# Performance work log

Hardware: AMD Instinct MI355X
Metric: run time of the kernel (lower is better)

Reference implementation:

```python
import jax, jax.numpy as jnp
import numpy as np

B, S, D = 2, 2048, 2048
H, HKV, HD = 16, 4, 128
GROUPS = H // HKV
SCALE = HD ** -0.5
ROPE_THETA = 10000.0
NEG = -1e9


def _rope_cos_sin():
    inv_freq = 1.0 / (ROPE_THETA ** (jnp.arange(0, HD, 2, dtype=jnp.float32) / HD))  # [HD/2]
    pos = jnp.arange(S, dtype=jnp.float32)
    freqs = pos[:, None] * inv_freq[None, :]            # [S, HD/2]
    emb = jnp.concatenate([freqs, freqs], axis=-1)      # [S, HD]
    cos = jnp.broadcast_to(jnp.cos(emb)[None], (B, S, HD))
    sin = jnp.broadcast_to(jnp.sin(emb)[None], (B, S, HD))
    return cos, sin


def setup_inputs() -> dict:
    key = jax.random.key(0)
    ks = jax.random.split(key, 5)
    hidden_states = jax.random.normal(ks[0], (B, S, D), dtype=jnp.float32)
    cos, sin = _rope_cos_sin()
    causal = jnp.where(jnp.arange(S)[:, None] >= jnp.arange(S)[None, :], 0.0, NEG).astype(jnp.float32)
    attn_mask = jnp.broadcast_to(causal[None, None], (B, 1, S, S))
    wq = jax.random.normal(ks[1], (H * HD, D), dtype=jnp.float32) * (D ** -0.5)
    wk = jax.random.normal(ks[2], (HKV * HD, D), dtype=jnp.float32) * (D ** -0.5)
    wv = jax.random.normal(ks[3], (HKV * HD, D), dtype=jnp.float32) * (D ** -0.5)
    wo = jax.random.normal(ks[4], (D, H * HD), dtype=jnp.float32) * (D ** -0.5)
    return {"hidden_states": hidden_states, "cos": cos, "sin": sin,
            "attn_mask": attn_mask, "wq": wq, "wk": wk, "wv": wv, "wo": wo}


def _rotate_half(x):
    x1, x2 = x[..., : HD // 2], x[..., HD // 2:]
    return jnp.concatenate([-x2, x1], axis=-1)


def reference(hidden_states, cos, sin, attn_mask, wq, wk, wv, wo):
    # projections (torch Linear: x @ W.T), reshape to [B, heads, S, HD]
    q = (hidden_states @ wq.T).reshape(B, S, H, HD).transpose(0, 2, 1, 3)
    k = (hidden_states @ wk.T).reshape(B, S, HKV, HD).transpose(0, 2, 1, 3)
    v = (hidden_states @ wv.T).reshape(B, S, HKV, HD).transpose(0, 2, 1, 3)
    # RoPE (cos/sin broadcast over head dim)
    c = cos[:, None, :, :]
    s = sin[:, None, :, :]
    q = q * c + _rotate_half(q) * s
    k = k * c + _rotate_half(k) * s
    # GQA: repeat each kv head GROUPS times consecutively (matches repeat_kv)
    k = jnp.repeat(k, GROUPS, axis=1)
    v = jnp.repeat(v, GROUPS, axis=1)
    logits = jnp.einsum('bhqd,bhkd->bhqk', q, k) * SCALE + attn_mask
    w = jax.nn.softmax(logits.astype(jnp.float32), axis=-1).astype(q.dtype)
    out = jnp.einsum('bhqk,bhkd->bhqd', w, v)            # [B,H,S,HD]
    out = out.transpose(0, 2, 1, 3).reshape(B, S, H * HD)
    return out @ wo.T
```

## Files before the change

kernel.cpp:

```cpp
#include <hip/hip_runtime.h>

typedef __attribute__((ext_vector_type(8))) short bf16x8;
typedef __attribute__((ext_vector_type(4))) float f32x4;
typedef __attribute__((ext_vector_type(16))) float f32x16;
typedef __attribute__((ext_vector_type(8))) unsigned short u16x8;
typedef __attribute__((ext_vector_type(4))) unsigned u32x4;
typedef unsigned short u16;

#define GLOBAL_AS __attribute__((address_space(1)))
#define LDS_AS __attribute__((address_space(3)))

#define S_ 2048
#define SMK_ 0.12751741406106783f

static __device__ __forceinline__ u16 f2bf(float f) {
  unsigned u = __builtin_bit_cast(unsigned, f);
  u += 0x7fffu + ((u >> 16) & 1u);
  return (u16)(u >> 16);
}
static __device__ __forceinline__ float bf2f(u16 h) {
  return __builtin_bit_cast(float, ((unsigned)h) << 16);
}
static __device__ __forceinline__ float exp2_raw(float x) {
  float r; asm("v_exp_f32 %0, %1" : "=v"(r) : "v"(x)); return r;
}
static __device__ __forceinline__ unsigned cvtpk(float lo, float hi_) {
  unsigned r; asm("v_cvt_pk_bf16_f32 %0, %1, %2" : "=v"(r) : "v"(lo), "v"(hi_)); return r;
}
static __device__ __forceinline__ float tmax16(const f32x16& s) {
  float a0 = fmaxf(s[0], s[1]),  a1 = fmaxf(s[2], s[3]);
  float a2 = fmaxf(s[4], s[5]),  a3 = fmaxf(s[6], s[7]);
  float a4 = fmaxf(s[8], s[9]),  a5 = fmaxf(s[10], s[11]);
  float a6 = fmaxf(s[12], s[13]), a7 = fmaxf(s[14], s[15]);
  return fmaxf(fmaxf(fmaxf(a0, a1), fmaxf(a2, a3)),
               fmaxf(fmaxf(a4, a5), fmaxf(a6, a7)));
}
static __device__ __forceinline__ float tsum16(const f32x16& s) {
  float a0 = s[0] + s[1],  a1 = s[2] + s[3];
  float a2 = s[4] + s[5],  a3 = s[6] + s[7];
  float a4 = s[8] + s[9],  a5 = s[10] + s[11];
  float a6 = s[12] + s[13], a7 = s[14] + s[15];
  return ((a0 + a1) + (a2 + a3)) + ((a4 + a5) + (a6 + a7));
}

__global__ __launch_bounds__(256)
void cvt_all(const float* __restrict__ h, const float* __restrict__ wq,
             const float* __restrict__ wk, const float* __restrict__ wv,
             const float* __restrict__ wo, u16* __restrict__ Xbf,
             u16* __restrict__ Wqkv, u16* __restrict__ Wo) {
  const int bid = blockIdx.x;
  const float* src; u16* dst; long base;
  if (bid < 4096)      { src = h;  dst = Xbf;            base = (long)bid * 2048; }
  else if (bid < 6144) { src = wq; dst = Wqkv;           base = (long)(bid - 4096) * 2048; }
  else if (bid < 6656) { src = wk; dst = Wqkv + 4194304; base = (long)(bid - 6144) * 2048; }
  else if (bid < 7168) { src = wv; dst = Wqkv + 5242880; base = (long)(bid - 6656) * 2048; }
  else                 { src = wo; dst = Wo;             base = (long)(bid - 7168) * 2048; }
  const long i = base + (long)threadIdx.x * 8;
  f32x4 a = *(const f32x4*)(src + i);
  f32x4 b = *(const f32x4*)(src + i + 4);
  u16x8 o;
  o[0] = f2bf(a[0]); o[1] = f2bf(a[1]); o[2] = f2bf(a[2]); o[3] = f2bf(a[3]);
  o[4] = f2bf(b[0]); o[5] = f2bf(b[1]); o[6] = f2bf(b[2]); o[7] = f2bf(b[3]);
  *(u16x8*)(dst + i) = o;
}

template <int NJ, bool BF16OUT>
__global__ __launch_bounds__(512, 2)
void gemm256(const u16* __restrict__ A, const u16* __restrict__ Bw,
             void* __restrict__ Cp, int M, int N, int K) {
  __shared__ u16 LA[4][2][4096];
  __shared__ u16 LB[4][NJ / 2][4096];

  const int tid = threadIdx.x;
  const int wave = tid >> 6, lane = tid & 63;
  const int fr = lane & 15, fg = lane >> 4;
  const int wm = (wave >> 2) * 128;
  const int wn = (wave & 3) * (NJ * 16);
  const long rowA = (long)blockIdx.y * 256;
  const long rowB = (long)blockIdx.x * (NJ * 64);

  const int srow = tid >> 2;
  const int sc8 = (tid & 3) ^ (srow & 3);
  const int wbase = wave * 512;

  const int nt = K >> 5;

  f32x4 acc[8][NJ] = {};

#define STAGE_A(pt)                                                          \
  {                                                                          \
    const int _b = (pt) & 3;                                                 \
    const long _k = (long)(pt) * 32 + sc8 * 8;                               \
    __builtin_amdgcn_global_load_lds(                                        \
        (GLOBAL_AS void*)(A + (rowA + srow) * K + _k),                       \
        (LDS_AS void*)(&LA[_b][0][wbase]), 16, 0, 0);                        \
    __builtin_amdgcn_global_load_lds(                                        \
        (GLOBAL_AS void*)(A + (rowA + 128 + srow) * K + _k),                 \
        (LDS_AS void*)(&LA[_b][1][wbase]), 16, 0, 0);                        \
  }
#define STAGE_B(pt)                                                          \
  {                                                                          \
    const int _b = (pt) & 3;                                                 \
    const long _k = (long)(pt) * 32 + sc8 * 8;                               \
    __builtin_amdgcn_global_load_lds(                                        \
        (GLOBAL_AS void*)(Bw + (rowB + srow) * K + _k),                      \
        (LDS_AS void*)(&LB[_b][0][wbase]), 16, 0, 0);                        \
    if (NJ == 4)                                                             \
      __builtin_amdgcn_global_load_lds(                                      \
          (GLOBAL_AS void*)(Bw + (rowB + 128 + srow) * K + _k),              \
          (LDS_AS void*)(&LB[_b][NJ / 2 - 1][wbase]), 16, 0, 0);             \
  }

  STAGE_A(0); STAGE_B(0);
  STAGE_A(1); STAGE_B(1);
  STAGE_A(2); STAGE_B(2);

  for (int t = 0; t < nt; ++t) {
    const int rem = nt - 1 - t;
    if (NJ == 4) {
      if (rem >= 2)      asm volatile("s_waitcnt vmcnt(8)" ::: "memory");
      else if (rem == 1) asm volatile("s_waitcnt vmcnt(4)" ::: "memory");
      else               asm volatile("s_waitcnt vmcnt(0)" ::: "memory");
    } else {
      if (rem >= 2)      asm volatile("s_waitcnt vmcnt(6)" ::: "memory");
      else if (rem == 1) asm volatile("s_waitcnt vmcnt(3)" ::: "memory");
      else               asm volatile("s_waitcnt vmcnt(0)" ::: "memory");
    }
    __builtin_amdgcn_s_barrier();

    const u16* Ah = LA[t & 3][wm >> 7];
    const u16* Bh = LB[t & 3][NJ == 4 ? (wn >> 7) : 0];
    const bool pf = (t + 3) < nt;

    bf16x8 af0[4], bfv[NJ];
#pragma unroll
    for (int mi = 0; mi < 4; ++mi) {
      const int rl = mi * 16 + fr;
      af0[mi] = *(const bf16x8*)&Ah[rl * 32 + ((fg ^ (rl & 3)) << 3)];
    }
#pragma unroll
    for (int nj = 0; nj < NJ; ++nj) {
      const int rb = (wn & 127) + nj * 16 + fr;
      bfv[nj] = *(const bf16x8*)&Bh[rb * 32 + ((fg ^ (rb & 3)) << 3)];
    }
    if (pf) STAGE_A(t + 3);
    __builtin_amdgcn_s_setprio(1);
#pragma unroll
    for (int mi = 0; mi < 4; ++mi)
#pragma unroll
      for (int nj = 0; nj < NJ; ++nj)
        acc[mi][nj] = __builtin_amdgcn_mfma_f32_16x16x32_bf16(af0[mi], bfv[nj], acc[mi][nj], 0, 0, 0);
    __builtin_amdgcn_s_setprio(0);

    bf16x8 af1[4];
#pragma unroll
    for (int mi = 0; mi < 4; ++mi) {
      const int rl = 64 + mi * 16 + fr;
      af1[mi] = *(const bf16x8*)&Ah[rl * 32 + ((fg ^ (rl & 3)) << 3)];
    }
    if (pf) STAGE_B(t + 3);
    __builtin_amdgcn_s_setprio(1);
#pragma unroll
    for (int mi = 0; mi < 4; ++mi)
#pragma unroll
      for (int nj = 0; nj < NJ; ++nj)
        acc[4 + mi][nj] = __builtin_amdgcn_mfma_f32_16x16x32_bf16(af1[mi], bfv[nj], acc[4 + mi][nj], 0, 0, 0);
    __builtin_amdgcn_s_setprio(0);

    __builtin_amdgcn_s_barrier();
  }
#undef STAGE_A
#undef STAGE_B

#pragma unroll
  for (int mi = 0; mi < 8; ++mi)
#pragma unroll
    for (int nj = 0; nj < NJ; ++nj)
#pragma unroll
      for (int r = 0; r < 4; ++r) {
        const long row = rowA + wm + mi * 16 + fg * 4 + r;
        const long col = rowB + wn + nj * 16 + fr;
        if (BF16OUT) ((u16*)Cp)[row * N + col] = f2bf(acc[mi][nj][r]);
        else         ((float*)Cp)[row * N + col] = acc[mi][nj][r];
      }
}

__global__ __launch_bounds__(256)
void rope_rearrange(const u16* __restrict__ QKV, const float* __restrict__ cosb,
                    const float* __restrict__ sinb, u16* __restrict__ Qr,
                    u16* __restrict__ Kr) {
  const int m = blockIdx.x;
  const int b = m >> 11, s = m & 2047;
  const int t = threadIdx.x;
  const u16* row = QKV + (long)m * 3072;
  const float* cp = cosb + (long)m * 128;
  const float* sp = sinb + (long)m * 128;
#pragma unroll
  for (int i = 0; i < 4; ++i) {
    const int idx = i * 256 + t;
    const int h = idx >> 6, d = idx & 63;
    const float x1 = bf2f(row[h * 128 + d]);
    const float x2 = bf2f(row[h * 128 + d + 64]);
    const float c = cp[d], sv = sp[d];
    const long o = ((long)(b * 16 + h) * S_ + s) * 128 + d;
    Qr[o] = f2bf(x1 * c - x2 * sv);
    Qr[o + 64] = f2bf(x2 * c + x1 * sv);
  }
  {
    const int h = t >> 6, d = t & 63;
    const float x1 = bf2f(row[2048 + h * 128 + d]);
    const float x2 = bf2f(row[2048 + h * 128 + d + 64]);
    const float c = cp[d], sv = sp[d];
    const long o = ((long)(b * 4 + h) * S_ + s) * 128 + d;
    Kr[o] = f2bf((x1 * c - x2 * sv) * SMK_);
    Kr[o + 64] = f2bf((x2 * c + x1 * sv) * SMK_);
  }
}

__global__ __launch_bounds__(256)
void transpose_v(const u16* __restrict__ QKV, u16* __restrict__ Vt) {
  __shared__ u16 t[32][33];
  const int s0 = blockIdx.x * 32, d0 = blockIdx.y * 32;
  const int bk = blockIdx.z;
  const int b = bk >> 2, kh = bk & 3;
  const int tx = threadIdx.x & 31, ty = threadIdx.x >> 5;
  const u16* src = QKV + 2560 + (long)kh * 128;
#pragma unroll
  for (int i = 0; i < 4; ++i) {
    const int sl = ty + i * 8;
    t[sl][tx] = src[(long)(b * S_ + s0 + sl) * 3072 + d0 + tx];
  }
  __syncthreads();
  u16* dst = Vt + (long)(b * 4 + kh) * 128 * S_;
#pragma unroll
  for (int i = 0; i < 4; ++i) {
    const int dl = ty + i * 8;
    dst[(long)(d0 + dl) * S_ + s0 + tx] = t[tx][dl];
  }
}

struct PA2 { bf16x8 a, b; };
static __device__ __forceinline__ PA2 pack_half(const f32x16 s) {
  PA2 out;
#pragma unroll
  for (int ks2 = 0; ks2 < 2; ++ks2) {
    const int rb = ks2 * 8;
    unsigned w0 = cvtpk(s[rb + 0], s[rb + 1]);
    unsigned w1 = cvtpk(s[rb + 2], s[rb + 3]);
    unsigned w2 = cvtpk(s[rb + 4], s[rb + 5]);
    unsigned w3 = cvtpk(s[rb + 6], s[rb + 7]);
    asm("v_permlane32_swap_b32 %0, %1" : "+v"(w0), "+v"(w2));
    asm("v_permlane32_swap_b32 %0, %1" : "+v"(w1), "+v"(w3));
    u32x4 pw; pw[0] = w0; pw[1] = w1; pw[2] = w2; pw[3] = w3;
    if (ks2 == 0) out.a = __builtin_bit_cast(bf16x8, pw);
    else          out.b = __builtin_bit_cast(bf16x8, pw);
  }
  return out;
}

template <int NH>
static __device__ __forceinline__ void attn_tile(
    const u16* __restrict__ Ks, const u16* __restrict__ Vs,
    const bf16x8 (&qf)[8], f32x16 (&acc)[4], float& m_run, float& l_run,
    const int kv0, const int qwmin, const int qg, const int l31,
    const int hi, const int r7) {
  f32x16 s[NH];
#pragma unroll
  for (int hh = 0; hh < NH; ++hh) s[hh] = (f32x16){};
  __builtin_amdgcn_s_setprio(1);
#pragma unroll
  for (int ds = 0; ds < 8; ++ds) {
    const int ch = ((2 * ds + hi) ^ r7) << 3;
#pragma unroll
    for (int hh = 0; hh < NH; ++hh) {
      const bf16x8 ka = *(const bf16x8*)&Ks[(hh * 32 + l31) * 128 + ch];
      s[hh] = __builtin_amdgcn_mfma_f32_32x32x16_bf16(ka, qf[ds], s[hh], 0, 0, 0);
    }
  }
  __builtin_amdgcn_s_setprio(0);

  if (kv0 + NH * 32 - 1 > qwmin) {
#pragma unroll
    for (int hh = 0; hh < NH; ++hh)
#pragma unroll
      for (int r = 0; r < 16; ++r) {
        const int cr = (r & 3) + 8 * (r >> 2) + 4 * hi;
        if (kv0 + hh * 32 + cr > qg) s[hh][r] = -3.0e38f;
      }
  }

  float mx = tmax16(s[0]);
  if (NH == 2) mx = fmaxf(mx, tmax16(s[1]));
  mx = fmaxf(mx, __shfl_xor(mx, 32));

  if (__any(mx > m_run + 8.0f)) {
    const float mn = fmaxf(m_run, mx);
    const float scq = exp2_raw(m_run - mn);
    m_run = mn; l_run *= scq;
#pragma unroll
    for (int r = 0; r < 16; ++r) {
      const int cr = (r & 3) + 8 * (r >> 2) + 4 * hi;
      const float sr = __shfl(scq, cr);
      acc[0][r] *= sr; acc[1][r] *= sr; acc[2][r] *= sr; acc[3][r] *= sr;
    }
  }

#pragma unroll
  for (int hh = 0; hh < NH; ++hh)
#pragma unroll
    for (int r = 0; r < 16; ++r) s[hh][r] = exp2_raw(s[hh][r] - m_run);
  float rs = tsum16(s[0]);
  if (NH == 2) rs += tsum16(s[1]);
  rs += __shfl_xor(rs, 32);
  l_run += rs;

  bf16x8 pa[2 * NH];
#pragma unroll
  for (int hh = 0; hh < NH; ++hh) {
    const PA2 p = pack_half(s[hh]);
    pa[2 * hh] = p.a; pa[2 * hh + 1] = p.b;
  }
  __builtin_amdgcn_s_setprio(1);
#pragma unroll
  for (int nj = 0; nj < 4; ++nj) {
    const int vrow = (nj * 32 + l31) * 64;
#pragma unroll
    for (int ks = 0; ks < 2 * NH; ++ks) {
      const bf16x8 vf = *(const bf16x8*)&Vs[vrow + (((2 * ks + hi) ^ r7) << 3)];
      acc[nj] = __builtin_amdgcn_mfma_f32_32x32x16_bf16(pa[ks], vf, acc[nj], 0, 0, 0);
    }
  }
  __builtin_amdgcn_s_setprio(0);
}

#define NUNITS 1024
__global__ __launch_bounds__(128)
void attn_fwd(const u16* __restrict__ Qr, const u16* __restrict__ Kr,
              const u16* __restrict__ Vt, u16* __restrict__ Att,
              unsigned* __restrict__ ctr) {
  __shared__ u16 Ks[64 * 128];
  __shared__ u16 Vs[128 * 64];
  __shared__ unsigned s_uid;

  const int tid = threadIdx.x, wave = tid >> 6, lane = tid & 63;
  const int l31 = lane & 31, hi = lane >> 5, r7 = lane & 7;

  for (;;) {
    __syncthreads();
    if (tid == 0) s_uid = atomicAdd(ctr, 1u);
    __syncthreads();
    const unsigned uid = s_uid;
    if (uid >= NUNITS) break;

    const int g = uid & 7;
    const int rem = uid >> 3;
    const int qt = 31 - (rem >> 2);
    const int b = g >> 2, kh = g & 3;
    const int h = kh * 4 + (rem & 3);
    const int qwmin = qt * 64 + wave * 32;

    const u16* Qb = Qr + (long)(b * 16 + h) * S_ * 128;
    const u16* Kb = Kr + (long)(b * 4 + kh) * S_ * 128;
    const u16* Vg = Vt + (long)(b * 4 + kh) * 128 * (long)S_;

    bf16x8 qf[8];
    const u16* qrow = Qb + (long)(qwmin + l31) * 128 + hi * 8;
#pragma unroll
    for (int ds = 0; ds < 8; ++ds) qf[ds] = *(const bf16x8*)(qrow + ds * 16);

    f32x16 acc[4] = {};
    float m_run = -1e30f, l_run = 0.f;
    const int qg = qwmin + l31;

    const int ntiles = qt + 1;
    for (int t = 0; t < ntiles; ++t) {
      const int kv0 = t * 64;
      __syncthreads();
#pragma unroll
      for (int c = 0; c < 8; ++c) {
        const int slab = wave * 8 + c;
        const int offu = slab * 512 + lane * 8;
        const int kvl = offu >> 7;
        const int kc = ((offu >> 3) & 15) ^ (kvl & 7);
        __builtin_amdgcn_global_load_lds(
            (GLOBAL_AS void*)(Kb + (long)(kv0 + kvl) * 128 + kc * 8),
            (LDS_AS void*)(Ks + slab * 512), 16, 0, 0);
        const int dr = offu >> 6;
        const int vc = ((offu >> 3) & 7) ^ (dr & 7);
        __builtin_amdgcn_global_load_lds(
            (GLOBAL_AS void*)(Vg + (long)dr * S_ + kv0 + vc * 8),
            (LDS_AS void*)(Vs + slab * 512), 16, 0, 0);
      }
      __syncthreads();

      if (kv0 + 32 <= qwmin + 31)
        attn_tile<2>(Ks, Vs, qf, acc, m_run, l_run, kv0, qwmin, qg, l31, hi, r7);
      else if (kv0 <= qwmin + 31)
        attn_tile<1>(Ks, Vs, qf, acc, m_run, l_run, kv0, qwmin, qg, l31, hi, r7);
    }

    const float inv = 1.0f / l_run;
#pragma unroll
    for (int r = 0; r < 16; ++r) {
      const int cr = (r & 3) + 8 * (r >> 2) + 4 * hi;
      const float ir = __shfl(inv, cr);
      const long orow = ((long)b * S_ + qt * 64 + wave * 32 + cr) * 2048 + h * 128 + l31;
      Att[orow]      = f2bf(acc[0][r] * ir);
      Att[orow + 32] = f2bf(acc[1][r] * ir);
      Att[orow + 64] = f2bf(acc[2][r] * ir);
      Att[orow + 96] = f2bf(acc[3][r] * ir);
    }
  }
}

extern "C" void kernel_launch(void* const* d_in, const int* in_sizes, int n_in,
                              void* d_out, int out_size, void* d_ws, size_t ws_size,
                              hipStream_t stream) {
  const float* hidden = (const float*)d_in[0];
  const float* cosb = (const float*)d_in[1];
  const float* sinb = (const float*)d_in[2];
  const float* wq = (const float*)d_in[4];
  const float* wk = (const float*)d_in[5];
  const float* wv = (const float*)d_in[6];
  const float* wo = (const float*)d_in[7];
  float* out = (float*)d_out;

  u16* Xbf  = (u16*)d_ws;
  u16* Wqkv = Xbf + 8388608;
  u16* Wo   = Wqkv + 6291456;
  u16* QKV  = Wo + 4194304;
  u16* Qr   = QKV + 12582912;
  u16* Kr   = Qr + 8388608;
  u16* Vtp  = Kr + 2097152;
  u16* Att  = Xbf;
  if (ws_size < (size_t)44040192 * 2) return;

  cvt_all<<<dim3(9216), dim3(256), 0, stream>>>(hidden, wq, wk, wv, wo, Xbf, Wqkv, Wo);
  gemm256<4, true><<<dim3(12, 16), dim3(512), 0, stream>>>(Xbf, Wqkv, (void*)QKV, 4096, 3072, 2048);
  rope_rearrange<<<dim3(4096), dim3(256), 0, stream>>>(QKV, cosb, sinb, Qr, Kr);
  transpose_v<<<dim3(64, 4, 8), dim3(256), 0, stream>>>(QKV, Vtp);
  hipMemsetAsync((void*)Wqkv, 0, 4, stream);
  attn_fwd<<<dim3(1024), dim3(128), 0, stream>>>(Qr, Kr, Vtp, Att, (unsigned*)Wqkv);
  gemm256<2, false><<<dim3(16, 16), dim3(512), 0, stream>>>(Att, Wo, (void*)out, 4096, 2048, 2048);
}
```

Baseline: 227.2 us.

## Use per-XCD work queues and 4-wave blocks sharing K/V tiles across head pairs

Replaces the single global work counter with eight per-(batch, kv-head) counters. Each block starts on the queue matching its XCC id, read via s_getreg, and falls back to the other queues when its own is empty, so K/V for a given kv head tends to stay in one XCD's L2. Blocks grow to 256 threads so two query heads sharing a kv head reuse each staged K/V tile in LDS, which halves the per-wave load work. The risks are coarser work units that may hurt load balance on the causal tail, and more atomic traffic when queues run dry.

```diff
diff --git a/kernel.cpp b/kernel.cpp
--- a/kernel.cpp
+++ b/kernel.cpp
@@ -333,11 +333,11 @@
   __builtin_amdgcn_s_setprio(0);
 }
 
-#define NUNITS 1024
-__global__ __launch_bounds__(128)
+#define PAIRS_PER_GRP 64u
+__global__ __launch_bounds__(256)
 void attn_fwd(const u16* __restrict__ Qr, const u16* __restrict__ Kr,
               const u16* __restrict__ Vt, u16* __restrict__ Att,
-              unsigned* __restrict__ ctr) {
+              unsigned* __restrict__ ctrs) {
   __shared__ u16 Ks[64 * 128];
   __shared__ u16 Vs[128 * 64];
   __shared__ unsigned s_uid;
@@ -345,19 +345,31 @@
   const int tid = threadIdx.x, wave = tid >> 6, lane = tid & 63;
   const int l31 = lane & 31, hi = lane >> 5, r7 = lane & 7;
 
+  const int xcc = __builtin_amdgcn_s_getreg(6164) & 7;
+
   for (;;) {
     __syncthreads();
-    if (tid == 0) s_uid = atomicAdd(ctr, 1u);
+    if (tid == 0) {
+      unsigned got = 0xffffffffu;
+#pragma unroll
+      for (int k = 0; k < 8; ++k) {
+        const int sq = (xcc + k) & 7;
+        const unsigned v = atomicAdd(&ctrs[sq], 1u);
+        if (v < PAIRS_PER_GRP) { got = (unsigned)sq * PAIRS_PER_GRP + v; break; }
+      }
+      s_uid = got;
+    }
     __syncthreads();
     const unsigned uid = s_uid;
-    if (uid >= NUNITS) break;
-
-    const int g = uid & 7;
-    const int rem = uid >> 3;
-    const int qt = 31 - (rem >> 2);
+    if (uid == 0xffffffffu) break;
+
+    const int g = uid >> 6;
+    const int u = uid & 63;
+    const int qt = 31 - (u >> 1);
+    const int hp = u & 1;
     const int b = g >> 2, kh = g & 3;
-    const int h = kh * 4 + (rem & 3);
-    const int qwmin = qt * 64 + wave * 32;
+    const int h = kh * 4 + hp * 2 + (wave >> 1);
+    const int qwmin = qt * 64 + (wave & 1) * 32;
 
     const u16* Qb = Qr + (long)(b * 16 + h) * S_ * 128;
     const u16* Kb = Kr + (long)(b * 4 + kh) * S_ * 128;
@@ -377,8 +389,8 @@
       const int kv0 = t * 64;
       __syncthreads();
 #pragma unroll
-      for (int c = 0; c < 8; ++c) {
-        const int slab = wave * 8 + c;
+      for (int c = 0; c < 4; ++c) {
+        const int slab = wave * 4 + c;
         const int offu = slab * 512 + lane * 8;
         const int kvl = offu >> 7;
         const int kc = ((offu >> 3) & 15) ^ (kvl & 7);
@@ -404,7 +416,7 @@
     for (int r = 0; r < 16; ++r) {
       const int cr = (r & 3) + 8 * (r >> 2) + 4 * hi;
       const float ir = __shfl(inv, cr);
-      const long orow = ((long)b * S_ + qt * 64 + wave * 32 + cr) * 2048 + h * 128 + l31;
+      const long orow = ((long)b * S_ + qwmin + cr) * 2048 + h * 128 + l31;
       Att[orow]      = f2bf(acc[0][r] * ir);
       Att[orow + 32] = f2bf(acc[1][r] * ir);
       Att[orow + 64] = f2bf(acc[2][r] * ir);
@@ -439,7 +451,7 @@
   gemm256<4, true><<<dim3(12, 16), dim3(512), 0, stream>>>(Xbf, Wqkv, (void*)QKV, 4096, 3072, 2048);
   rope_rearrange<<<dim3(4096), dim3(256), 0, stream>>>(QKV, cosb, sinb, Qr, Kr);
   transpose_v<<<dim3(64, 4, 8), dim3(256), 0, stream>>>(QKV, Vtp);
-  hipMemsetAsync((void*)Wqkv, 0, 4, stream);
-  attn_fwd<<<dim3(1024), dim3(128), 0, stream>>>(Qr, Kr, Vtp, Att, (unsigned*)Wqkv);
+  hipMemsetAsync((void*)Wqkv, 0, 32, stream);
+  attn_fwd<<<dim3(512), dim3(256), 0, stream>>>(Qr, Kr, Vtp, Att, (unsigned*)Wqkv);
   gemm256<2, false><<<dim3(16, 16), dim3(512), 0, stream>>>(Att, Wo, (void*)out, 4096, 2048, 2048);
 }
```

Result: slower. 257.4 us (+13.3%).

## Load K/V directly from global into registers in single-wave attention blocks

Applied to the files above, without the earlier changes.

The attention kernel drops LDS staging and the persistent atomic work queue. Each 64-thread block now handles one 32-row query strip and reads K and V fragments straight from global memory into registers, relying on cache reuse across the four heads sharing a KV head. This removes barriers and LDS traffic and allows higher occupancy via launch bounds. The cost is redundant global/L2 reads, and static scheduling in place of dynamic load balancing across the causal triangle.

```diff
diff --git a/kernel.cpp b/kernel.cpp
--- a/kernel.cpp
+++ b/kernel.cpp
@@ -259,25 +259,34 @@
 }
 
 template <int NH>
-static __device__ __forceinline__ void attn_tile(
-    const u16* __restrict__ Ks, const u16* __restrict__ Vs,
+static __device__ __forceinline__ void attn_tile_g(
+    const u16* __restrict__ Kb, const u16* __restrict__ Vg,
     const bf16x8 (&qf)[8], f32x16 (&acc)[4], float& m_run, float& l_run,
-    const int kv0, const int qwmin, const int qg, const int l31,
-    const int hi, const int r7) {
+    const int kv0, const int qwmin, const int qg, const int l31, const int hi) {
   f32x16 s[NH];
 #pragma unroll
   for (int hh = 0; hh < NH; ++hh) s[hh] = (f32x16){};
-  __builtin_amdgcn_s_setprio(1);
-#pragma unroll
-  for (int ds = 0; ds < 8; ++ds) {
-    const int ch = ((2 * ds + hi) ^ r7) << 3;
-#pragma unroll
-    for (int hh = 0; hh < NH; ++hh) {
-      const bf16x8 ka = *(const bf16x8*)&Ks[(hh * 32 + l31) * 128 + ch];
-      s[hh] = __builtin_amdgcn_mfma_f32_32x32x16_bf16(ka, qf[ds], s[hh], 0, 0, 0);
-    }
-  }
-  __builtin_amdgcn_s_setprio(0);
+  const u16* kr0 = Kb + (long)(kv0 + l31) * 128 + hi * 8;
+  {
+    bf16x8 ka[8];
+#pragma unroll
+    for (int ds = 0; ds < 8; ++ds) ka[ds] = *(const bf16x8*)(kr0 + ds * 16);
+    __builtin_amdgcn_s_setprio(1);
+#pragma unroll
+    for (int ds = 0; ds < 8; ++ds)
+      s[0] = __builtin_amdgcn_mfma_f32_32x32x16_bf16(ka[ds], qf[ds], s[0], 0, 0, 0);
+    __builtin_amdgcn_s_setprio(0);
+  }
+  if (NH == 2) {
+    bf16x8 ka[8];
+#pragma unroll
+    for (int ds = 0; ds < 8; ++ds) ka[ds] = *(const bf16x8*)(kr0 + 32 * 128 + ds * 16);
+    __builtin_amdgcn_s_setprio(1);
+#pragma unroll
+    for (int ds = 0; ds < 8; ++ds)
+      s[NH - 1] = __builtin_amdgcn_mfma_f32_32x32x16_bf16(ka[ds], qf[ds], s[NH - 1], 0, 0, 0);
+    __builtin_amdgcn_s_setprio(0);
+  }
 
   if (kv0 + NH * 32 - 1 > qwmin) {
 #pragma unroll
@@ -320,96 +329,71 @@
     const PA2 p = pack_half(s[hh]);
     pa[2 * hh] = p.a; pa[2 * hh + 1] = p.b;
   }
+
   __builtin_amdgcn_s_setprio(1);
 #pragma unroll
   for (int nj = 0; nj < 4; ++nj) {
-    const int vrow = (nj * 32 + l31) * 64;
-#pragma unroll
-    for (int ks = 0; ks < 2 * NH; ++ks) {
-      const bf16x8 vf = *(const bf16x8*)&Vs[vrow + (((2 * ks + hi) ^ r7) << 3)];
-      acc[nj] = __builtin_amdgcn_mfma_f32_32x32x16_bf16(pa[ks], vf, acc[nj], 0, 0, 0);
+    const u16* vr = Vg + (long)(nj * 32 + l31) * S_ + kv0 + hi * 8;
+    const bf16x8 vf0 = *(const bf16x8*)(vr);
+    const bf16x8 vf1 = *(const bf16x8*)(vr + 16);
+    acc[nj] = __builtin_amdgcn_mfma_f32_32x32x16_bf16(pa[0], vf0, acc[nj], 0, 0, 0);
+    acc[nj] = __builtin_amdgcn_mfma_f32_32x32x16_bf16(pa[1], vf1, acc[nj], 0, 0, 0);
+    if (NH == 2) {
+      const bf16x8 vf2 = *(const bf16x8*)(vr + 32);
+      const bf16x8 vf3 = *(const bf16x8*)(vr + 48);
+      acc[nj] = __builtin_amdgcn_mfma_f32_32x32x16_bf16(pa[2 * NH - 2], vf2, acc[nj], 0, 0, 0);
+      acc[nj] = __builtin_amdgcn_mfma_f32_32x32x16_bf16(pa[2 * NH - 1], vf3, acc[nj], 0, 0, 0);
     }
   }
   __builtin_amdgcn_s_setprio(0);
 }
 
-#define NUNITS 1024
-__global__ __launch_bounds__(128)
+__global__ __launch_bounds__(64, 3)
 void attn_fwd(const u16* __restrict__ Qr, const u16* __restrict__ Kr,
-              const u16* __restrict__ Vt, u16* __restrict__ Att,
-              unsigned* __restrict__ ctr) {
-  __shared__ u16 Ks[64 * 128];
-  __shared__ u16 Vs[128 * 64];
-  __shared__ unsigned s_uid;
-
-  const int tid = threadIdx.x, wave = tid >> 6, lane = tid & 63;
-  const int l31 = lane & 31, hi = lane >> 5, r7 = lane & 7;
-
-  for (;;) {
-    __syncthreads();
-    if (tid == 0) s_uid = atomicAdd(ctr, 1u);
-    __syncthreads();
-    const unsigned uid = s_uid;
-    if (uid >= NUNITS) break;
-
-    const int g = uid & 7;
-    const int rem = uid >> 3;
-    const int qt = 31 - (rem >> 2);
-    const int b = g >> 2, kh = g & 3;
-    const int h = kh * 4 + (rem & 3);
-    const int qwmin = qt * 64 + wave * 32;
-
-    const u16* Qb = Qr + (long)(b * 16 + h) * S_ * 128;
-    const u16* Kb = Kr + (long)(b * 4 + kh) * S_ * 128;
-    const u16* Vg = Vt + (long)(b * 4 + kh) * 128 * (long)S_;
-
-    bf16x8 qf[8];
-    const u16* qrow = Qb + (long)(qwmin + l31) * 128 + hi * 8;
-#pragma unroll
-    for (int ds = 0; ds < 8; ++ds) qf[ds] = *(const bf16x8*)(qrow + ds * 16);
-
-    f32x16 acc[4] = {};
-    float m_run = -1e30f, l_run = 0.f;
-    const int qg = qwmin + l31;
-
-    const int ntiles = qt + 1;
-    for (int t = 0; t < ntiles; ++t) {
-      const int kv0 = t * 64;
-      __syncthreads();
-#pragma unroll
-      for (int c = 0; c < 8; ++c) {
-        const int slab = wave * 8 + c;
-        const int offu = slab * 512 + lane * 8;
-        const int kvl = offu >> 7;
-        const int kc = ((offu >> 3) & 15) ^ (kvl & 7);
-        __builtin_amdgcn_global_load_lds(
-            (GLOBAL_AS void*)(Kb + (long)(kv0 + kvl) * 128 + kc * 8),
-            (LDS_AS void*)(Ks + slab * 512), 16, 0, 0);
-        const int dr = offu >> 6;
-        const int vc = ((offu >> 3) & 7) ^ (dr & 7);
-        __builtin_amdgcn_global_load_lds(
-            (GLOBAL_AS void*)(Vg + (long)dr * S_ + kv0 + vc * 8),
-            (LDS_AS void*)(Vs + slab * 512), 16, 0, 0);
-      }
-      __syncthreads();
-
-      if (kv0 + 32 <= qwmin + 31)
-        attn_tile<2>(Ks, Vs, qf, acc, m_run, l_run, kv0, qwmin, qg, l31, hi, r7);
-      else if (kv0 <= qwmin + 31)
-        attn_tile<1>(Ks, Vs, qf, acc, m_run, l_run, kv0, qwmin, qg, l31, hi, r7);
-    }
-
-    const float inv = 1.0f / l_run;
-#pragma unroll
-    for (int r = 0; r < 16; ++r) {
-      const int cr = (r & 3) + 8 * (r >> 2) + 4 * hi;
-      const float ir = __shfl(inv, cr);
-      const long orow = ((long)b * S_ + qt * 64 + wave * 32 + cr) * 2048 + h * 128 + l31;
-      Att[orow]      = f2bf(acc[0][r] * ir);
-      Att[orow + 32] = f2bf(acc[1][r] * ir);
-      Att[orow + 64] = f2bf(acc[2][r] * ir);
-      Att[orow + 96] = f2bf(acc[3][r] * ir);
-    }
+              const u16* __restrict__ Vt, u16* __restrict__ Att) {
+  const int lane = threadIdx.x & 63;
+  const int l31 = lane & 31, hi = lane >> 5;
+
+  const int uid = blockIdx.x;
+  const int g = uid >> 8;
+  const int r = uid & 255;
+  const int qw = 63 - (r >> 2);
+  const int b = g >> 2, kh = g & 3;
+  const int h = kh * 4 + (r & 3);
+  const int qwmin = qw * 32;
+
+  const u16* Qb = Qr + (long)(b * 16 + h) * S_ * 128;
+  const u16* Kb = Kr + (long)(b * 4 + kh) * S_ * 128;
+  const u16* Vg = Vt + (long)(b * 4 + kh) * 128 * (long)S_;
+
+  bf16x8 qf[8];
+  const u16* qrow = Qb + (long)(qwmin + l31) * 128 + hi * 8;
+#pragma unroll
+  for (int ds = 0; ds < 8; ++ds) qf[ds] = *(const bf16x8*)(qrow + ds * 16);
+
+  f32x16 acc[4] = {};
+  float m_run = -1e30f, l_run = 0.f;
+  const int qg = qwmin + l31;
+
+  const int ntiles = (qw >> 1) + 1;
+  for (int t = 0; t < ntiles; ++t) {
+    const int kv0 = t * 64;
+    if (kv0 + 32 <= qwmin + 31)
+      attn_tile_g<2>(Kb, Vg, qf, acc, m_run, l_run, kv0, qwmin, qg, l31, hi);
+    else
+      attn_tile_g<1>(Kb, Vg, qf, acc, m_run, l_run, kv0, qwmin, qg, l31, hi);
+  }
+
+  const float inv = 1.0f / l_run;
+#pragma unroll
+  for (int r2 = 0; r2 < 16; ++r2) {
+    const int cr = (r2 & 3) + 8 * (r2 >> 2) + 4 * hi;
+    const float ir = __shfl(inv, cr);
+    const long orow = ((long)b * S_ + qwmin + cr) * 2048 + h * 128 + l31;
+    Att[orow]      = f2bf(acc[0][r2] * ir);
+    Att[orow + 32] = f2bf(acc[1][r2] * ir);
+    Att[orow + 64] = f2bf(acc[2][r2] * ir);
+    Att[orow + 96] = f2bf(acc[3][r2] * ir);
   }
 }
 
@@ -439,7 +423,6 @@
   gemm256<4, true><<<dim3(12, 16), dim3(512), 0, stream>>>(Xbf, Wqkv, (void*)QKV, 4096, 3072, 2048);
   rope_rearrange<<<dim3(4096), dim3(256), 0, stream>>>(QKV, cosb, sinb, Qr, Kr);
   transpose_v<<<dim3(64, 4, 8), dim3(256), 0, stream>>>(QKV, Vtp);
-  hipMemsetAsync((void*)Wqkv, 0, 4, stream);
-  attn_fwd<<<dim3(1024), dim3(128), 0, stream>>>(Qr, Kr, Vtp, Att, (unsigned*)Wqkv);
+  attn_fwd<<<dim3(2048), dim3(64), 0, stream>>>(Qr, Kr, Vtp, Att);
   gemm256<2, false><<<dim3(16, 16), dim3(512), 0, stream>>>(Att, Wo, (void*)out, 4096, 2048, 2048);
 }
```

Measured after the change: 506.4 us. +122.8%, slower.
